# Performance work log

Hardware: AMD Instinct MI355X
Metric: run time of the kernel (lower is better)

The kernel has to match this reference:

```python
import jax, jax.numpy as jnp
import numpy as np

WINDOW = 128
LOOK_BACKWARD = 1
LOOK_FORWARD = 0  # causal
PAD_VALUE = -1
MASK_VALUE = -jnp.finfo(jnp.float32).max


def look_around(x, backward=LOOK_BACKWARD, forward=LOOK_FORWARD, pad_value=PAD_VALUE):
    # x: [b, w, n, ...] -> [b, w, (backward+forward+1)*n, ...]
    w = x.shape[1]
    pad_width = [(0, 0)] * x.ndim
    pad_width[1] = (backward, forward)
    p = jnp.pad(x, pad_width, constant_values=pad_value)
    return jnp.concatenate([p[:, i:i + w] for i in range(backward + forward + 1)], axis=2)


def rotate_half(x):
    x1, x2 = jnp.split(x, 2, axis=-1)
    return jnp.concatenate([-x2, x1], axis=-1)


def setup_inputs() -> dict:
    key = jax.random.key(0)
    k1, k2, k3 = jax.random.split(key, 3)
    shape = (8, 4, 4096, 64)
    q = jax.random.normal(k1, shape, dtype=jnp.float32)
    k = jax.random.normal(k2, shape, dtype=jnp.float32)
    v = jax.random.normal(k3, shape, dtype=jnp.float32)
    bin_attention_mask = jnp.ones((8, 4096), dtype=jnp.int32)
    return {"q": q, "k": k, "v": v, "bin_attention_mask": bin_attention_mask}


def reference(q, k, v, bin_attention_mask):
    B, H, n, d = q.shape
    b = B * H
    qf = q.reshape(b, n, d)
    kf = k.reshape(b, n, d)
    vf = v.reshape(b, n, d)

    # sinusoidal rotary embedding (rel_pos_emb_dim == d)
    inv_freq = 1.0 / (10000.0 ** (jnp.arange(0, d, 2, dtype=jnp.float32) / d))
    t = jnp.arange(n, dtype=jnp.float32)
    freqs = jnp.einsum('i,j->ij', t, inv_freq)          # [n, d/2]
    freqs = jnp.concatenate([freqs, freqs], axis=-1)     # [n, d]
    cos, sin = jnp.cos(freqs), jnp.sin(freqs)
    qf = qf * cos + rotate_half(qf) * sin
    kf = kf * cos + rotate_half(kf) * sin

    scale = d ** -0.5
    w = n // WINDOW
    bq = qf.reshape(b, w, WINDOW, d)
    bk = look_around(kf.reshape(b, w, WINDOW, d), pad_value=float(PAD_VALUE))
    bv = look_around(vf.reshape(b, w, WINDOW, d), pad_value=float(PAD_VALUE))

    seq = jnp.arange(n, dtype=jnp.int32).reshape(1, w, WINDOW)
    bq_t = seq[..., :, None]                              # [1, w, i, 1]
    bq_k = look_around(seq)[..., None, :]                 # [1, w, 1, j]

    sim = jnp.einsum('bwie,bwje->bwij', bq, bk) * scale   # [b, w, i, j]

    causal_mask = bq_t < bq_k
    sim = jnp.where(causal_mask, MASK_VALUE, sim)

    # binary attention mask: [B, n] -> [B, w, 2*WINDOW] -> broadcast over heads
    m = bin_attention_mask.astype(bool).reshape(B, w, WINDOW)
    m = look_around(m, pad_value=False)                   # [B, w, j]
    m = jnp.repeat(m, H, axis=0)[:, :, None, :]           # [(B H), w, 1, j]
    sim = jnp.where(~m, MASK_VALUE, sim)

    attn = jax.nn.softmax(sim, axis=-1)
    out = jnp.einsum('bwij,bwje->bwie', attn, bv)
    return out.reshape(B, H, n, d)
```

## Files before the change

kernel.cpp:

```cpp
#include <hip/hip_runtime.h>

typedef __attribute__((ext_vector_type(8))) short bf16x8;
typedef __attribute__((ext_vector_type(4))) short bf16x4;
typedef __attribute__((ext_vector_type(4))) float f32x4;
typedef unsigned int u32;
typedef unsigned short u16;
typedef unsigned long long u64;

#define NSEQ 4096
#define DD   64
#define NEG  3.0e4f
#define L32  0.4152410118609203f

__device__ __forceinline__ u16 f2bf(float f) {
    union { float f; u32 i; } x; x.f = f;
    u32 r = x.i + 0x7fffu + ((x.i >> 16) & 1u);
    return (u16)(r >> 16);
}

__device__ __forceinline__ void stage_k(int tid, int bh, int gkbase, int hibase,
                                        const float* __restrict__ K,
                                        u16 (*Kb)[72],
                                        const float2 (*tabLo)[64],
                                        const float2 (*tabHi)[32])
{
    const int r = tid >> 2, qt = tid & 3, e0 = qt * 16;
    const int gk = gkbase + r;
    u16 y[16] __attribute__((aligned(16)));
    if (gk >= 0) {
        const float* kp = K + (size_t)(bh * NSEQ + gk) * DD;
        float a[16], b[16];
        #pragma unroll
        for (int i = 0; i < 4; ++i) {
            *(float4*)&a[i * 4] = *(const float4*)(kp + e0 + i * 4);
            *(float4*)&b[i * 4] = *(const float4*)(kp + (e0 ^ 32) + i * 4);
        }
        const int lo = gk & 63, h = (gk >> 6) - hibase;
        const float sgn = (e0 < 32) ? -1.f : 1.f;
        const int i0 = e0 & 31;
        #pragma unroll
        for (int jj = 0; jj < 16; ++jj) {
            float2 L = tabLo[i0 + jj][lo];
            float2 H = tabHi[h][i0 + jj];
            float cc = H.x * L.x - H.y * L.y;
            float ss = H.y * L.x + H.x * L.y;
            y[jj] = f2bf(a[jj] * cc + sgn * b[jj] * ss);
        }
    } else {
        #pragma unroll
        for (int jj = 0; jj < 16; ++jj) y[jj] = 0;
    }
    *(uint4*)&Kb[r][e0]     = ((const uint4*)y)[0];
    *(uint4*)&Kb[r][e0 + 8] = ((const uint4*)y)[1];
}

__global__ __launch_bounds__(512) void lattn(
    const float* __restrict__ Q, const float* __restrict__ K,
    const float* __restrict__ V, const int* __restrict__ M,
    float* __restrict__ O)
{
    __shared__ u16 Kb[128][72];
    __shared__ u16 Vt[64][264];
    __shared__ u16 Ps[8][16][40];
    __shared__ __align__(16) float2 tabLo[32][64];
    __shared__ float2 tabHi[4][32];

    const int w = blockIdx.x, bh = blockIdx.y, batch = bh >> 2;
    const int tid = threadIdx.x, lane = tid & 63, wv = tid >> 6;
    const int kbase = w * 128 - 128;
    const int hibase = (kbase > 0 ? kbase : 0) >> 6;
    const int m_ = lane & 15, qd = lane >> 4;
    const int rb = wv * 16;
    const int tq = w * 128 + rb + m_;

    {
        const int e = tid * 4, fi = e >> 6, lo = e & 63;
        const float th = exp2f(-(float)fi * L32);
        float2 t4[4];
        #pragma unroll
        for (int s = 0; s < 4; ++s) {
            float sv, cv;
            sincosf((float)(lo + s) * th, &sv, &cv);
            t4[s] = make_float2(cv, sv);
        }
        *(float4*)&tabLo[fi][lo]     = *(float4*)&t4[0];
        *(float4*)&tabLo[fi][lo + 2] = *(float4*)&t4[2];
        if (tid < 128) {
            const int h = tid >> 5, f2 = tid & 31;
            const float th2 = exp2f(-(float)f2 * L32);
            float sv, cv;
            sincosf((float)((hibase + h) * 64) * th2, &sv, &cv);
            tabHi[h][f2] = make_float2(cv, sv);
        }
    }

    u64 vb[4];
    #pragma unroll
    for (int i = 0; i < 4; ++i) {
        int gk = kbase + i * 64 + lane;
        int mv = (gk >= 0) ? M[batch * NSEQ + gk] : 0;
        vb[i] = __ballot(mv != 0);
    }

    {
        const int j = tid >> 1, h = tid & 1, gk = kbase + j;
        float rv[32];
        if (gk >= 0) {
            const float* vr = V + (size_t)(bh * NSEQ + gk) * DD + h * 32;
            #pragma unroll
            for (int i = 0; i < 8; ++i) *(float4*)&rv[i * 4] = *(const float4*)(vr + i * 4);
        } else {
            #pragma unroll
            for (int i = 0; i < 32; ++i) rv[i] = 0.f;
        }
        #pragma unroll
        for (int i = 0; i < 32; ++i) Vt[h * 32 + i][j] = f2bf(rv[i]);
    }

    __syncthreads();

    stage_k(tid, bh, kbase, hibase, K, Kb, tabLo, tabHi);

    bf16x8 qf0, qf1;
    {
        const float* qr = Q + (size_t)(bh * NSEQ + tq) * DD;
        float ql[8], qh_[8];
        *(float4*)&ql[0]  = *(const float4*)(qr + qd * 8);
        *(float4*)&ql[4]  = *(const float4*)(qr + qd * 8 + 4);
        *(float4*)&qh_[0] = *(const float4*)(qr + qd * 8 + 32);
        *(float4*)&qh_[4] = *(const float4*)(qr + qd * 8 + 36);
        const int qlo = tq & 63, qh = (tq >> 6) - hibase;
        #pragma unroll
        for (int jj = 0; jj < 8; ++jj) {
            const int fi = qd * 8 + jj;
            float2 L = tabLo[fi][qlo];
            float2 H = tabHi[qh][fi];
            float cc = H.x * L.x - H.y * L.y;
            float ss = H.y * L.x + H.x * L.y;
            qf0[jj] = (short)f2bf(ql[jj]  * cc - qh_[jj] * ss);
            qf1[jj] = (short)f2bf(qh_[jj] * cc + ql[jj]  * ss);
        }
    }

    __syncthreads();

    f32x4 acc[16];
    const f32x4 zf = {0.f, 0.f, 0.f, 0.f};
    #pragma unroll
    for (int t = 0; t < 8; ++t) {
        bf16x8 kf0 = *(const bf16x8*)&Kb[t * 16 + m_][qd * 8];
        bf16x8 kf1 = *(const bf16x8*)&Kb[t * 16 + m_][32 + qd * 8];
        f32x4 c0 = __builtin_amdgcn_mfma_f32_16x16x32_bf16(kf0, qf0, zf, 0, 0, 0);
        acc[t]   = __builtin_amdgcn_mfma_f32_16x16x32_bf16(kf1, qf1, c0, 0, 0, 0);
    }

    __syncthreads();

    stage_k(tid, bh, kbase + 128, hibase, K, Kb, tabLo, tabHi);

    __syncthreads();

    #pragma unroll
    for (int t = 8; t < 16; ++t) {
        bf16x8 kf0 = *(const bf16x8*)&Kb[(t - 8) * 16 + m_][qd * 8];
        bf16x8 kf1 = *(const bf16x8*)&Kb[(t - 8) * 16 + m_][32 + qd * 8];
        f32x4 c0 = __builtin_amdgcn_mfma_f32_16x16x32_bf16(kf0, qf0, zf, 0, 0, 0);
        acc[t]   = __builtin_amdgcn_mfma_f32_16x16x32_bf16(kf1, qf1, c0, 0, 0, 0);
    }

    const int lim = tq - kbase;
    float mx = -NEG;
    #pragma unroll
    for (int t = 0; t < 16; ++t)
        #pragma unroll
        for (int r = 0; r < 4; ++r) {
            int nn = t * 16 + qd * 4 + r;
            bool ok = (nn <= lim) && ((vb[t >> 2] >> (nn & 63)) & 1ull);
            float s = ok ? acc[t][r] * 0.125f : -NEG;
            acc[t][r] = s;
            mx = fmaxf(mx, s);
        }
    mx = fmaxf(mx, __shfl_xor(mx, 16));
    mx = fmaxf(mx, __shfl_xor(mx, 32));
    float sum = 0.f;
    #pragma unroll
    for (int t = 0; t < 16; ++t)
        #pragma unroll
        for (int r = 0; r < 4; ++r) {
            float p = __expf(acc[t][r] - mx);
            acc[t][r] = p; sum += p;
        }
    sum += __shfl_xor(sum, 16);
    sum += __shfl_xor(sum, 32);
    const float is = 1.f / sum;

    f32x4 o[4] = {zf, zf, zf, zf};
    #pragma unroll
    for (int kc = 0; kc < 8; ++kc) {
        bf16x4 w0, w1;
        #pragma unroll
        for (int r = 0; r < 4; ++r) {
            w0[r] = (short)f2bf(acc[2 * kc][r] * is);
            w1[r] = (short)f2bf(acc[2 * kc + 1][r] * is);
        }
        *(bf16x4*)&Ps[wv][m_][qd * 4]      = w0;
        *(bf16x4*)&Ps[wv][m_][16 + qd * 4] = w1;
        __builtin_amdgcn_sched_barrier(0);
        bf16x8 pf = *(const bf16x8*)&Ps[wv][m_][qd * 8];
        __builtin_amdgcn_sched_barrier(0);
        #pragma unroll
        for (int et = 0; et < 4; ++et) {
            bf16x8 vf = *(const bf16x8*)&Vt[et * 16 + m_][kc * 32 + qd * 8];
            o[et] = __builtin_amdgcn_mfma_f32_16x16x32_bf16(pf, vf, o[et], 0, 0, 0);
        }
    }

    float* ob = O + (size_t)(bh * NSEQ + w * 128 + rb + qd * 4) * DD;
    #pragma unroll
    for (int r = 0; r < 4; ++r)
        #pragma unroll
        for (int et = 0; et < 4; ++et)
            ob[r * DD + et * 16 + m_] = o[et][r];
}

extern "C" void kernel_launch(void* const* d_in, const int* in_sizes, int n_in,
                              void* d_out, int out_size, void* d_ws, size_t ws_size,
                              hipStream_t stream) {
    const float* q = (const float*)d_in[0];
    const float* k = (const float*)d_in[1];
    const float* v = (const float*)d_in[2];
    const int*   m = (const int*)d_in[3];
    float* o = (float*)d_out;
    dim3 grid(32, 32);
    lattn<<<grid, 512, 0, stream>>>(q, k, v, m, o);
}
```

Measured before the change: 153.4 us.

## Precompute global RoPE table, swizzle LDS, stage full K window once, defer softmax normalization

```diff
diff --git a/kernel.cpp b/kernel.cpp
--- a/kernel.cpp
+++ b/kernel.cpp
@@ -1,98 +1,49 @@
 #include <hip/hip_runtime.h>
 
 typedef __attribute__((ext_vector_type(8))) short bf16x8;
-typedef __attribute__((ext_vector_type(4))) short bf16x4;
 typedef __attribute__((ext_vector_type(4))) float f32x4;
 typedef unsigned int u32;
 typedef unsigned short u16;
 typedef unsigned long long u64;
 
-#define NSEQ 4096
-#define DD   64
-#define NEG  3.0e4f
-#define L32  0.4152410118609203f
-
-__device__ __forceinline__ u16 f2bf(float f) {
-    union { float f; u32 i; } x; x.f = f;
-    u32 r = x.i + 0x7fffu + ((x.i >> 16) & 1u);
-    return (u16)(r >> 16);
-}
-
-__device__ __forceinline__ void stage_k(int tid, int bh, int gkbase, int hibase,
-                                        const float* __restrict__ K,
-                                        u16 (*Kb)[72],
-                                        const float2 (*tabLo)[64],
-                                        const float2 (*tabHi)[32])
-{
-    const int r = tid >> 2, qt = tid & 3, e0 = qt * 16;
-    const int gk = gkbase + r;
-    u16 y[16] __attribute__((aligned(16)));
-    if (gk >= 0) {
-        const float* kp = K + (size_t)(bh * NSEQ + gk) * DD;
-        float a[16], b[16];
-        #pragma unroll
-        for (int i = 0; i < 4; ++i) {
-            *(float4*)&a[i * 4] = *(const float4*)(kp + e0 + i * 4);
-            *(float4*)&b[i * 4] = *(const float4*)(kp + (e0 ^ 32) + i * 4);
-        }
-        const int lo = gk & 63, h = (gk >> 6) - hibase;
-        const float sgn = (e0 < 32) ? -1.f : 1.f;
-        const int i0 = e0 & 31;
-        #pragma unroll
-        for (int jj = 0; jj < 16; ++jj) {
-            float2 L = tabLo[i0 + jj][lo];
-            float2 H = tabHi[h][i0 + jj];
-            float cc = H.x * L.x - H.y * L.y;
-            float ss = H.y * L.x + H.x * L.y;
-            y[jj] = f2bf(a[jj] * cc + sgn * b[jj] * ss);
-        }
-    } else {
-        #pragma unroll
-        for (int jj = 0; jj < 16; ++jj) y[jj] = 0;
-    }
-    *(uint4*)&Kb[r][e0]     = ((const uint4*)y)[0];
-    *(uint4*)&Kb[r][e0 + 8] = ((const uint4*)y)[1];
-}
-
-__global__ __launch_bounds__(512) void lattn(
+#define NSEQ  4096
+#define DD    64
+#define NFREQ 32
+#define NEG   3.0e4f
+#define L32   0.4152410118609203f
+
+__device__ float2 g_tab[NSEQ * NFREQ];
+
+__global__ __launch_bounds__(512) void rope_tab() {
+    const int i = blockIdx.x * 512 + threadIdx.x;
+    const int pos = i >> 5, fi = i & 31;
+    const float th = exp2f(-(float)fi * L32);
+    float s, c;
+    sincosf((float)pos * th, &s, &c);
+    g_tab[i] = make_float2(c, s);
+}
+
+__device__ __forceinline__ u32 pkbf(float lo, float hi) {
+    u32 r;
+    asm("v_cvt_pk_bf16_f32 %0, %1, %2" : "=v"(r) : "v"(lo), "v"(hi));
+    return r;
+}
+
+__global__ __launch_bounds__(512, 4) void lattn(
     const float* __restrict__ Q, const float* __restrict__ K,
     const float* __restrict__ V, const int* __restrict__ M,
     float* __restrict__ O)
 {
-    __shared__ u16 Kb[128][72];
-    __shared__ u16 Vt[64][264];
-    __shared__ u16 Ps[8][16][40];
-    __shared__ __align__(16) float2 tabLo[32][64];
-    __shared__ float2 tabHi[4][32];
+    __shared__ __align__(16) u16 Kb[256 * 64];
+    __shared__ __align__(16) u16 Vt[64 * 256];
+    __shared__ __align__(16) u16 Ps[8][512];
 
     const int w = blockIdx.x, bh = blockIdx.y, batch = bh >> 2;
     const int tid = threadIdx.x, lane = tid & 63, wv = tid >> 6;
     const int kbase = w * 128 - 128;
-    const int hibase = (kbase > 0 ? kbase : 0) >> 6;
     const int m_ = lane & 15, qd = lane >> 4;
     const int rb = wv * 16;
     const int tq = w * 128 + rb + m_;
-
-    {
-        const int e = tid * 4, fi = e >> 6, lo = e & 63;
-        const float th = exp2f(-(float)fi * L32);
-        float2 t4[4];
-        #pragma unroll
-        for (int s = 0; s < 4; ++s) {
-            float sv, cv;
-            sincosf((float)(lo + s) * th, &sv, &cv);
-            t4[s] = make_float2(cv, sv);
-        }
-        *(float4*)&tabLo[fi][lo]     = *(float4*)&t4[0];
-        *(float4*)&tabLo[fi][lo + 2] = *(float4*)&t4[2];
-        if (tid < 128) {
-            const int h = tid >> 5, f2 = tid & 31;
-            const float th2 = exp2f(-(float)f2 * L32);
-            float sv, cv;
-            sincosf((float)((hibase + h) * 64) * th2, &sv, &cv);
-            tabHi[h][f2] = make_float2(cv, sv);
-        }
-    }
 
     u64 vb[4];
     #pragma unroll
@@ -103,69 +54,115 @@
     }
 
     {
-        const int j = tid >> 1, h = tid & 1, gk = kbase + j;
-        float rv[32];
+        const int kp = tid >> 2, qt = tid & 3;
+        const int gk0 = kbase + 2 * kp;
+        float v0[16] __attribute__((aligned(16)));
+        float v1[16] __attribute__((aligned(16)));
+        if (gk0 >= 0) {
+            const float* vr = V + (size_t)(bh * NSEQ + gk0) * DD + qt * 16;
+            #pragma unroll
+            for (int i = 0; i < 4; ++i) {
+                *(float4*)&v0[i * 4] = *(const float4*)(vr + i * 4);
+                *(float4*)&v1[i * 4] = *(const float4*)(vr + DD + i * 4);
+            }
+        } else {
+            #pragma unroll
+            for (int i = 0; i < 16; ++i) { v0[i] = 0.f; v1[i] = 0.f; }
+        }
+        char* vtb = (char*)Vt + (kp & 3) * 4;
+        const u32 c0 = (u32)(kp >> 2);
+        #pragma unroll
+        for (int i = 0; i < 16; ++i) {
+            const int d = qt * 16 + i;
+            const u32 swz = (u32)((d ^ (d >> 3)) & 7);
+            *(u32*)(vtb + d * 512 + ((c0 ^ swz) << 4)) = pkbf(v0[i], v1[i]);
+        }
+    }
+
+    {
+        const int r = tid >> 1, q2 = tid & 1, f0 = q2 * 16;
+        const int gk = kbase + r;
+        u32 ol[8] __attribute__((aligned(16)));
+        u32 oh[8] __attribute__((aligned(16)));
         if (gk >= 0) {
-            const float* vr = V + (size_t)(bh * NSEQ + gk) * DD + h * 32;
-            #pragma unroll
-            for (int i = 0; i < 8; ++i) *(float4*)&rv[i * 4] = *(const float4*)(vr + i * 4);
+            const float* kr = K + (size_t)(bh * NSEQ + gk) * DD + f0;
+            float a[16] __attribute__((aligned(16)));
+            float b[16] __attribute__((aligned(16)));
+            #pragma unroll
+            for (int i = 0; i < 4; ++i) {
+                *(float4*)&a[i * 4] = *(const float4*)(kr + i * 4);
+                *(float4*)&b[i * 4] = *(const float4*)(kr + 32 + i * 4);
+            }
+            float2 cs[16] __attribute__((aligned(16)));
+            const float2* tp = g_tab + gk * NFREQ + f0;
+            #pragma unroll
+            for (int i = 0; i < 8; ++i)
+                *(float4*)&cs[i * 2] = *(const float4*)(tp + i * 2);
+            #pragma unroll
+            for (int j = 0; j < 8; ++j) {
+                float l0 = a[2*j]   * cs[2*j].x   - b[2*j]   * cs[2*j].y;
+                float l1 = a[2*j+1] * cs[2*j+1].x - b[2*j+1] * cs[2*j+1].y;
+                float h0 = b[2*j]   * cs[2*j].x   + a[2*j]   * cs[2*j].y;
+                float h1 = b[2*j+1] * cs[2*j+1].x + a[2*j+1] * cs[2*j+1].y;
+                ol[j] = pkbf(l0, l1);
+                oh[j] = pkbf(h0, h1);
+            }
         } else {
             #pragma unroll
-            for (int i = 0; i < 32; ++i) rv[i] = 0.f;
-        }
-        #pragma unroll
-        for (int i = 0; i < 32; ++i) Vt[h * 32 + i][j] = f2bf(rv[i]);
-    }
-
-    __syncthreads();
-
-    stage_k(tid, bh, kbase, hibase, K, Kb, tabLo, tabHi);
+            for (int j = 0; j < 8; ++j) { ol[j] = 0u; oh[j] = 0u; }
+        }
+        char* kb = (char*)Kb + r * 128;
+        const u32 cb = ((u32)(2 * q2) ^ (u32)(r & 7)) << 4;
+        *(uint4*)(kb + (cb ^ 0u))  = *(uint4*)&ol[0];
+        *(uint4*)(kb + (cb ^ 16u)) = *(uint4*)&ol[4];
+        *(uint4*)(kb + (cb ^ 64u)) = *(uint4*)&oh[0];
+        *(uint4*)(kb + (cb ^ 80u)) = *(uint4*)&oh[4];
+    }
 
     bf16x8 qf0, qf1;
     {
-        const float* qr = Q + (size_t)(bh * NSEQ + tq) * DD;
-        float ql[8], qh_[8];
-        *(float4*)&ql[0]  = *(const float4*)(qr + qd * 8);
-        *(float4*)&ql[4]  = *(const float4*)(qr + qd * 8 + 4);
-        *(float4*)&qh_[0] = *(const float4*)(qr + qd * 8 + 32);
-        *(float4*)&qh_[4] = *(const float4*)(qr + qd * 8 + 36);
-        const int qlo = tq & 63, qh = (tq >> 6) - hibase;
-        #pragma unroll
-        for (int jj = 0; jj < 8; ++jj) {
-            const int fi = qd * 8 + jj;
-            float2 L = tabLo[fi][qlo];
-            float2 H = tabHi[qh][fi];
-            float cc = H.x * L.x - H.y * L.y;
-            float ss = H.y * L.x + H.x * L.y;
-            qf0[jj] = (short)f2bf(ql[jj]  * cc - qh_[jj] * ss);
-            qf1[jj] = (short)f2bf(qh_[jj] * cc + ql[jj]  * ss);
-        }
+        const float* qr = Q + (size_t)(bh * NSEQ + tq) * DD + qd * 8;
+        float ql[8]  __attribute__((aligned(16)));
+        float qh_[8] __attribute__((aligned(16)));
+        *(float4*)&ql[0]  = *(const float4*)(qr);
+        *(float4*)&ql[4]  = *(const float4*)(qr + 4);
+        *(float4*)&qh_[0] = *(const float4*)(qr + 32);
+        *(float4*)&qh_[4] = *(const float4*)(qr + 36);
+        float2 cs[8] __attribute__((aligned(16)));
+        const float2* tp = g_tab + tq * NFREQ + qd * 8;
+        #pragma unroll
+        for (int i = 0; i < 4; ++i)
+            *(float4*)&cs[i * 2] = *(const float4*)(tp + i * 2);
+        u32 w0[4] __attribute__((aligned(16)));
+        u32 w1[4] __attribute__((aligned(16)));
+        #pragma unroll
+        for (int j = 0; j < 4; ++j) {
+            float c0 = cs[2*j].x   * 0.125f, s0 = cs[2*j].y   * 0.125f;
+            float c1 = cs[2*j+1].x * 0.125f, s1 = cs[2*j+1].y * 0.125f;
+            w0[j] = pkbf(ql[2*j]  * c0 - qh_[2*j]  * s0,
+                         ql[2*j+1]* c1 - qh_[2*j+1]* s1);
+            w1[j] = pkbf(qh_[2*j]  * c0 + ql[2*j]  * s0,
+                         qh_[2*j+1]* c1 + ql[2*j+1]* s1);
+        }
+        qf0 = *(bf16x8*)w0;
+        qf1 = *(bf16x8*)w1;
     }
 
     __syncthreads();
 
     f32x4 acc[16];
     const f32x4 zf = {0.f, 0.f, 0.f, 0.f};
-    #pragma unroll
-    for (int t = 0; t < 8; ++t) {
-        bf16x8 kf0 = *(const bf16x8*)&Kb[t * 16 + m_][qd * 8];
-        bf16x8 kf1 = *(const bf16x8*)&Kb[t * 16 + m_][32 + qd * 8];
-        f32x4 c0 = __builtin_amdgcn_mfma_f32_16x16x32_bf16(kf0, qf0, zf, 0, 0, 0);
-        acc[t]   = __builtin_amdgcn_mfma_f32_16x16x32_bf16(kf1, qf1, c0, 0, 0, 0);
-    }
-
-    __syncthreads();
-
-    stage_k(tid, bh, kbase + 128, hibase, K, Kb, tabLo, tabHi);
-
-    __syncthreads();
-
-    #pragma unroll
-    for (int t = 8; t < 16; ++t) {
-        bf16x8 kf0 = *(const bf16x8*)&Kb[(t - 8) * 16 + m_][qd * 8];
-        bf16x8 kf1 = *(const bf16x8*)&Kb[(t - 8) * 16 + m_][32 + qd * 8];
-        f32x4 c0 = __builtin_amdgcn_mfma_f32_16x16x32_bf16(kf0, qf0, zf, 0, 0, 0);
-        acc[t]   = __builtin_amdgcn_mfma_f32_16x16x32_bf16(kf1, qf1, c0, 0, 0, 0);
+    {
+        const u32 co = ((u32)(qd ^ (m_ & 7))) << 4;
+        const char* kb0 = (const char*)Kb + m_ * 128 + co;
+        const char* kb1 = (const char*)Kb + m_ * 128 + (co ^ 64u);
+        #pragma unroll
+        for (int t = 0; t < 16; ++t) {
+            bf16x8 kf0 = *(const bf16x8*)(kb0 + t * 2048);
+            bf16x8 kf1 = *(const bf16x8*)(kb1 + t * 2048);
+            f32x4 c0 = __builtin_amdgcn_mfma_f32_16x16x32_bf16(kf0, qf0, zf, 0, 0, 0);
+            acc[t]   = __builtin_amdgcn_mfma_f32_16x16x32_bf16(kf1, qf1, c0, 0, 0, 0);
+        }
     }
 
     const int lim = tq - kbase;
@@ -176,7 +173,7 @@
         for (int r = 0; r < 4; ++r) {
             int nn = t * 16 + qd * 4 + r;
             bool ok = (nn <= lim) && ((vb[t >> 2] >> (nn & 63)) & 1ull);
-            float s = ok ? acc[t][r] * 0.125f : -NEG;
+            float s = ok ? acc[t][r] : -NEG;
             acc[t][r] = s;
             mx = fmaxf(mx, s);
         }
@@ -190,37 +187,55 @@
             float p = __expf(acc[t][r] - mx);
             acc[t][r] = p; sum += p;
         }
+
+    f32x4 o[4] = {zf, zf, zf, zf};
+    {
+        const u32 wbase = (u32)(wv * 1024 + m_ * 64);
+        const u32 ch0 = ((((u32)qd >> 1) ^ (u32)(m_ & 3)) << 4);
+        char* pw0 = (char*)Ps + wbase + (qd & 1) * 8 + ch0;
+        char* pw1 = (char*)Ps + wbase + (qd & 1) * 8 + (ch0 ^ 32u);
+        const char* pr = (const char*)Ps + wbase +
+                         (((u32)qd ^ (u32)(m_ & 3)) << 4);
+        const char* vbase[4];
+        u32 vxo[4];
+        #pragma unroll
+        for (int et = 0; et < 4; ++et) {
+            const int d = et * 16 + m_;
+            const u32 swz = (u32)((d ^ (d >> 3)) & 7);
+            vbase[et] = (const char*)Vt + d * 512 + (((u32)qd ^ (swz & 3u)) << 4);
+            vxo[et] = (swz >> 2) << 6;
+        }
+        #pragma unroll
+        for (int kc = 0; kc < 8; ++kc) {
+            u32 p0 = pkbf(acc[2*kc][0],   acc[2*kc][1]);
+            u32 p1 = pkbf(acc[2*kc][2],   acc[2*kc][3]);
+            u32 p2 = pkbf(acc[2*kc+1][0], acc[2*kc+1][1]);
+            u32 p3 = pkbf(acc[2*kc+1][2], acc[2*kc+1][3]);
+            *(uint2*)pw0 = make_uint2(p0, p1);
+            *(uint2*)pw1 = make_uint2(p2, p3);
+            __builtin_amdgcn_sched_barrier(0);
+            bf16x8 pf = *(const bf16x8*)pr;
+            __builtin_amdgcn_sched_barrier(0);
+            #pragma unroll
+            for (int et = 0; et < 4; ++et) {
+                bf16x8 vf = *(const bf16x8*)(vbase[et] + (((u32)(kc << 6)) ^ vxo[et]));
+                o[et] = __builtin_amdgcn_mfma_f32_16x16x32_bf16(pf, vf, o[et], 0, 0, 0);
+            }
+        }
+    }
+
     sum += __shfl_xor(sum, 16);
     sum += __shfl_xor(sum, 32);
     const float is = 1.f / sum;
-
-    f32x4 o[4] = {zf, zf, zf, zf};
-    #pragma unroll
-    for (int kc = 0; kc < 8; ++kc) {
-        bf16x4 w0, w1;
-        #pragma unroll
-        for (int r = 0; r < 4; ++r) {
-            w0[r] = (short)f2bf(acc[2 * kc][r] * is);
-            w1[r] = (short)f2bf(acc[2 * kc + 1][r] * is);
-        }
-        *(bf16x4*)&Ps[wv][m_][qd * 4]      = w0;
-        *(bf16x4*)&Ps[wv][m_][16 + qd * 4] = w1;
-        __builtin_amdgcn_sched_barrier(0);
-        bf16x8 pf = *(const bf16x8*)&Ps[wv][m_][qd * 8];
-        __builtin_amdgcn_sched_barrier(0);
-        #pragma unroll
-        for (int et = 0; et < 4; ++et) {
-            bf16x8 vf = *(const bf16x8*)&Vt[et * 16 + m_][kc * 32 + qd * 8];
-            o[et] = __builtin_amdgcn_mfma_f32_16x16x32_bf16(pf, vf, o[et], 0, 0, 0);
-        }
-    }
-
+    float isq[4];
+    #pragma unroll
+    for (int r = 0; r < 4; ++r) isq[r] = __shfl(is, qd * 4 + r);
     float* ob = O + (size_t)(bh * NSEQ + w * 128 + rb + qd * 4) * DD;
     #pragma unroll
     for (int r = 0; r < 4; ++r)
         #pragma unroll
         for (int et = 0; et < 4; ++et)
-            ob[r * DD + et * 16 + m_] = o[et][r];
+            ob[r * DD + et * 16 + m_] = o[et][r] * isq[r];
 }
 
 extern "C" void kernel_launch(void* const* d_in, const int* in_sizes, int n_in,
@@ -231,6 +246,7 @@
     const float* v = (const float*)d_in[2];
     const int*   m = (const int*)d_in[3];
     float* o = (float*)d_out;
+    rope_tab<<<dim3(NSEQ * NFREQ / 512), 512, 0, stream>>>();
     dim3 grid(32, 32);
     lattn<<<grid, 512, 0, stream>>>(q, k, v, m, o);
 }
```

After: 156.1 us. No clear change (+1.7%).
